# Kernel tuning notes

Hardware: AMD Instinct MI355X
Metric: run time of the kernel (lower is better)

The kernel has to match this reference:

```python
import jax, jax.numpy as jnp
import numpy as np

OUT_FEAT = 11008
IN_FEAT = 4096
HAD_DIM = 128


def setup_inputs() -> dict:
    key = jax.random.key(0)
    k1, k2, k3 = jax.random.split(key, 3)
    inp = jax.random.normal(k1, (OUT_FEAT, IN_FEAT), dtype=jnp.float32) * 0.02
    # rotation matrices (Hadamard-like random orthogonal stand-ins, scaled)
    R_left = jax.random.normal(k2, (IN_FEAT, IN_FEAT), dtype=jnp.float32) / np.sqrt(IN_FEAT)
    R_right = jax.random.normal(k3, (HAD_DIM, HAD_DIM), dtype=jnp.float32) / np.sqrt(HAD_DIM)
    return {"inp": inp, "R_left": R_left, "R_right": R_right}


def _fake_quant_int8(x):
    # symmetric per-tensor int8 fake quant with straight-through estimator
    scale = jnp.max(jnp.abs(x)) / 127.0
    scale = jnp.maximum(scale, jnp.finfo(x.dtype).tiny)
    q = jnp.clip(jnp.round(x / scale), -127.0, 127.0) * scale
    return x + jax.lax.stop_gradient(q - x)


def reference(inp, R_left, R_right):
    # RotQuantWrapper.forward, branch: R_left is not None, R1_is_left=True, R_right set.
    org_dtype = inp.dtype
    out_feat, in_feat = inp.shape  # inp is W^T: (out_feat, in_feat)
    compute_dtype = jnp.float32
    # inp @ R_left  -> (out_feat, in_feat)
    x = inp.astype(compute_dtype) @ R_left.astype(compute_dtype)
    had_dim = R_right.shape[0]
    # (W^T A)^T -> reshape -> block-multiply by B (had_dim blocks) -> back
    x = x.T  # (in_feat, out_feat)
    x = x.reshape(in_feat, out_feat // had_dim, had_dim)
    x = x @ R_right.astype(compute_dtype)  # batched small matmul over 128-blocks
    x = x.reshape(in_feat, out_feat).T  # (out_feat, in_feat)
    x = x.astype(org_dtype)
    return _fake_quant_int8(x)
```

## Files before the change

kernel.cpp:

```cpp
#include <hip/hip_runtime.h>
#include <hip/hip_fp16.h>

#define OUT_FEAT 11008
#define IN_FEAT  4096
#define HAD      128

typedef __attribute__((ext_vector_type(8))) _Float16 f16x8;
typedef __attribute__((ext_vector_type(4))) float    f32x4;

__device__ __forceinline__ void lds_load16(const _Float16* g, _Float16* l) {
    __builtin_amdgcn_global_load_lds(
        (const __attribute__((address_space(1))) void*)g,
        (__attribute__((address_space(3))) void*)l, 16, 0, 0);
}

__global__ __launch_bounds__(256, 2) void k_prep(const float* __restrict__ Rl,
                                                 const float* __restrict__ Rr,
                                                 const float* __restrict__ inp,
                                                 _Float16* __restrict__ Bt,
                                                 __half* __restrict__ W) {
    __shared__ char smem[65536];
    int bid = blockIdx.x;
    int t   = threadIdx.x;

    if (bid < 4096) {
        float (*tile)[65] = (float(*)[65])smem;
        int n0 = (bid & 63) * 64;
        int k0 = (bid >> 6) * 64;
        int tn = t & 63;
        int tr = t >> 6;
#pragma unroll
        for (int r = 0; r < 16; ++r) {
            int kk = r * 4 + tr;
            tile[kk][tn] = Rl[(size_t)(k0 + kk) * IN_FEAT + n0 + tn];
        }
        __syncthreads();
#pragma unroll
        for (int r = 0; r < 16; ++r) {
            int nn = r * 4 + tr;
            Bt[(size_t)(n0 + nn) * IN_FEAT + k0 + tn] = (_Float16)tile[tn][nn];
        }
        return;
    }

    __half2* sR2 = (__half2*)smem;
    __half2* sX2 = (__half2*)(smem + 32768);
    int rb = bid - 4096;
    int i0 = (rb & 31) * 128;
    int b  = rb >> 5;

#pragma unroll
    for (int r = 0; r < 32; ++r) {
        int idx = r * 256 + t;
        float2 v = *(const float2*)&Rr[(size_t)idx * 2];
        sR2[idx] = __floats2half2_rn(v.x, v.y);
    }
    const float* xsrc = inp + (size_t)b * HAD * IN_FEAT + i0;
#pragma unroll
    for (int r = 0; r < 32; ++r) {
        int idx = r * 256 + t;
        int k = idx >> 6, ip = idx & 63;
        float2 v = *(const float2*)&xsrc[(size_t)k * IN_FEAT + ip * 2];
        sX2[idx] = __floats2half2_rn(v.x, v.y);
    }
    __syncthreads();

    int tx = t & 15, ty = t >> 4;
    __half2 acc2[8][4];
#pragma unroll
    for (int j = 0; j < 8; ++j)
#pragma unroll
        for (int c = 0; c < 4; ++c) acc2[j][c] = __float2half2_rn(0.f);

    for (int k = 0; k < 128; ++k) {
        const __half2* rp = &sR2[k * 64 + ty * 4];
        __half2 rr[4] = {rp[0], rp[1], rp[2], rp[3]};
        const __half2* xp = &sX2[k * 64 + tx * 4];
        __half2 xv[4] = {xp[0], xp[1], xp[2], xp[3]};
#pragma unroll
        for (int q = 0; q < 4; ++q) {
            __half2 rlo = __low2half2(rr[q]);
            __half2 rhi = __high2half2(rr[q]);
#pragma unroll
            for (int c = 0; c < 4; ++c) {
                acc2[2 * q][c]     = __hfma2(rlo, xv[c], acc2[2 * q][c]);
                acc2[2 * q + 1][c] = __hfma2(rhi, xv[c], acc2[2 * q + 1][c]);
            }
        }
    }

#pragma unroll
    for (int jj = 0; jj < 8; ++jj) {
        size_t row = (size_t)(b * HAD + ty * 8 + jj) * IN_FEAT;
        union { __half2 h2[4]; f16x8 v; } u;
#pragma unroll
        for (int c = 0; c < 4; ++c) u.h2[c] = acc2[jj][c];
        *(f16x8*)&W[row + i0 + tx * 8] = u.v;
    }
}

#define BM 256
#define BN 256
#define BK 64
#define NT 64

#define DSA(dst, MH, KS, BUF)                                                 \
  _Pragma("unroll") for (int i_ = 0; i_ < 4; ++i_)                            \
      dst[i_] = *(const f16x8*)(aBase + (BUF)*16384 + ((MH)*4 + i_)*1024 +    \
                                ((KS) ? pk1 : pk0));

#define DSB(dst, KS, BUF)                                                     \
  _Pragma("unroll") for (int i_ = 0; i_ < 4; ++i_)                            \
      dst[i_] = *(const f16x8*)(bBase + (BUF)*16384 + i_*1024 +               \
                                ((KS) ? pk1 : pk0));

#define MFMAQ(AB, ar, br)                                                     \
  _Pragma("unroll") for (int mi_ = 0; mi_ < 4; ++mi_)                         \
  _Pragma("unroll") for (int ni_ = 0; ni_ < 4; ++ni_)                         \
      acc[(AB) + mi_][ni_] = __builtin_amdgcn_mfma_f32_16x16x32_f16(          \
          ar[mi_], br[ni_], acc[(AB) + mi_][ni_], 0, 0, 0);

#define PHEAD __builtin_amdgcn_s_barrier(); __builtin_amdgcn_s_setprio(1);
#define PTAIL __builtin_amdgcn_s_setprio(0); __builtin_amdgcn_s_barrier();

#define KTILE(BUF, MODE)                                                      \
  DSA(a, 0, 0, BUF) DSB(b0, 0, BUF)                                           \
  if ((MODE) >= 1) { lds_load16(pA00, &sA[(BUF)^1][0][dstOff]);               \
                     lds_load16(pA01, &sA[(BUF)^1][0][4096 + dstOff]); }      \
  PHEAD MFMAQ(0, a, b0) PTAIL                                                 \
  DSA(a, 0, 1, BUF) DSB(b1, 1, BUF)                                           \
  if ((MODE) >= 1) { lds_load16(pA10, &sA[(BUF)^1][1][dstOff]);               \
                     lds_load16(pA11, &sA[(BUF)^1][1][4096 + dstOff]);        \
                     pA00 += 64; pA01 += 64; pA10 += 64; pA11 += 64; }        \
  PHEAD MFMAQ(0, a, b1) PTAIL                                                 \
  DSA(a, 1, 0, BUF)                                                           \
  if ((MODE) == 2) { lds_load16(pB00, &sB[(BUF)][0][dstOff]);                 \
                     lds_load16(pB01, &sB[(BUF)][0][4096 + dstOff]); }        \
  PHEAD MFMAQ(4, a, b0) PTAIL                                                 \
  DSA(a, 1, 1, BUF)                                                           \
  if ((MODE) == 2) { lds_load16(pB10, &sB[(BUF)][1][dstOff]);                 \
                     lds_load16(pB11, &sB[(BUF)][1][4096 + dstOff]);          \
                     pB00 += 64; pB01 += 64; pB10 += 64; pB11 += 64; }        \
  __builtin_amdgcn_s_barrier(); __builtin_amdgcn_s_setprio(1);                \
  MFMAQ(4, a, b1)                                                             \
  __builtin_amdgcn_s_setprio(0);                                              \
  if ((MODE) == 2) asm volatile("s_waitcnt vmcnt(4)" ::: "memory");           \
  if ((MODE) == 1) asm volatile("s_waitcnt vmcnt(0)" ::: "memory");           \
  __builtin_amdgcn_s_barrier();

__global__ __launch_bounds__(512, 2) void k_gemm(const _Float16* __restrict__ A,
                                                 const _Float16* __restrict__ B,
                                                 float* __restrict__ Cf,
                                                 _Float16* __restrict__ Ch,
                                                 int zf16,
                                                 unsigned* __restrict__ absmax) {
    __shared__ _Float16 sA[2][2][8192];
    __shared__ _Float16 sB[2][2][8192];

    int obid = blockIdx.x;
    int bid  = (obid & 7) * 86 + (obid >> 3);
    int m0 = (bid >> 4) * BM;
    int n0 = (bid & 15) * BN;

    int t = threadIdx.x, lane = t & 63, wid = t >> 6;
    int wr = wid >> 2, wc = wid & 3;
    int fr = lane & 15, g = lane >> 4;

    int r0 = t >> 3;
    int cs = ((t & 7) ^ (r0 & 7)) * 8;
    size_t so = (size_t)r0 * IN_FEAT + cs;
    const _Float16* pA00 = A + (size_t)m0 * IN_FEAT + so;
    const _Float16* pA01 = pA00 + (size_t)64 * IN_FEAT;
    const _Float16* pA10 = pA00 + (size_t)128 * IN_FEAT;
    const _Float16* pA11 = pA00 + (size_t)192 * IN_FEAT;
    const _Float16* pB00 = B + (size_t)n0 * IN_FEAT + so;
    const _Float16* pB01 = pB00 + (size_t)64 * IN_FEAT;
    const _Float16* pB10 = pB00 + (size_t)128 * IN_FEAT;
    const _Float16* pB11 = pB00 + (size_t)192 * IN_FEAT;
    int dstOff = wid * 512;

    const _Float16* aBase = &sA[0][0][0] + wr * 8192 + fr * 64;
    const _Float16* bBase = &sB[0][0][0] + (wc >> 1) * 8192 + (wc & 1) * 4096 + fr * 64;
    int pk0 = (g ^ (fr & 7)) * 8;
    int pk1 = ((4 | g) ^ (fr & 7)) * 8;

    f32x4 acc[8][4] = {};
    f16x8 a[4], b0[4], b1[4];

    lds_load16(pB00, &sB[0][0][dstOff]); lds_load16(pB01, &sB[0][0][4096 + dstOff]);
    lds_load16(pB10, &sB[0][1][dstOff]); lds_load16(pB11, &sB[0][1][4096 + dstOff]);
    pB00 += 64; pB01 += 64; pB10 += 64; pB11 += 64;
    lds_load16(pA00, &sA[0][0][dstOff]); lds_load16(pA01, &sA[0][0][4096 + dstOff]);
    lds_load16(pA10, &sA[0][1][dstOff]); lds_load16(pA11, &sA[0][1][4096 + dstOff]);
    pA00 += 64; pA01 += 64; pA10 += 64; pA11 += 64;
    lds_load16(pB00, &sB[1][0][dstOff]); lds_load16(pB01, &sB[1][0][4096 + dstOff]);
    lds_load16(pB10, &sB[1][1][dstOff]); lds_load16(pB11, &sB[1][1][4096 + dstOff]);
    pB00 += 64; pB01 += 64; pB10 += 64; pB11 += 64;
    asm volatile("s_waitcnt vmcnt(4)" ::: "memory");
    __builtin_amdgcn_s_barrier();

#pragma unroll 1
    for (int kt = 0; kt < NT - 2; kt += 2) {
        KTILE(0, 2)
        KTILE(1, 2)
    }
    KTILE(0, 1)
    KTILE(1, 0)

    float mx = 0.f;
    if (zf16) {
#pragma unroll
        for (int mi = 0; mi < 8; ++mi) {
            int row_base = m0 + wr * 128 + mi * 16 + g * 4;
#pragma unroll
            for (int ni = 0; ni < 4; ++ni) {
                int col = n0 + wc * 64 + ni * 16 + fr;
#pragma unroll
                for (int r = 0; r < 4; ++r) {
                    _Float16 h = (_Float16)acc[mi][ni][r];
                    mx = fmaxf(mx, fabsf((float)h));
                    Ch[(size_t)(row_base + r) * IN_FEAT + col] = h;
                }
            }
        }
    } else {
#pragma unroll
        for (int mi = 0; mi < 8; ++mi) {
            int row_base = m0 + wr * 128 + mi * 16 + g * 4;
#pragma unroll
            for (int ni = 0; ni < 4; ++ni) {
                int col = n0 + wc * 64 + ni * 16 + fr;
#pragma unroll
                for (int r = 0; r < 4; ++r) {
                    float v = acc[mi][ni][r];
                    mx = fmaxf(mx, fabsf(v));
                    Cf[(size_t)(row_base + r) * IN_FEAT + col] = v;
                }
            }
        }
    }
#pragma unroll
    for (int off = 32; off; off >>= 1) mx = fmaxf(mx, __shfl_xor(mx, off));
    if (lane == 0) atomicMax(absmax, __float_as_uint(mx));
}

__global__ void k_quant_f16(const _Float16* __restrict__ Z, float* __restrict__ out,
                            const unsigned* __restrict__ absmax, int n8) {
    float amax  = __uint_as_float(*absmax);
    float scale = fmaxf(amax / 127.0f, 1.17549435e-38f);
    float inv   = 1.0f / scale;
    int stride = gridDim.x * blockDim.x;
    for (int i = blockIdx.x * blockDim.x + threadIdx.x; i < n8; i += stride) {
        f16x8 v = *(const f16x8*)&Z[(size_t)i * 8];
        float4 o1, o2;
        o1.x = fminf(127.f, fmaxf(-127.f, rintf((float)v[0] * inv))) * scale;
        o1.y = fminf(127.f, fmaxf(-127.f, rintf((float)v[1] * inv))) * scale;
        o1.z = fminf(127.f, fmaxf(-127.f, rintf((float)v[2] * inv))) * scale;
        o1.w = fminf(127.f, fmaxf(-127.f, rintf((float)v[3] * inv))) * scale;
        o2.x = fminf(127.f, fmaxf(-127.f, rintf((float)v[4] * inv))) * scale;
        o2.y = fminf(127.f, fmaxf(-127.f, rintf((float)v[5] * inv))) * scale;
        o2.z = fminf(127.f, fmaxf(-127.f, rintf((float)v[6] * inv))) * scale;
        o2.w = fminf(127.f, fmaxf(-127.f, rintf((float)v[7] * inv))) * scale;
        ((float4*)out)[i * 2]     = o1;
        ((float4*)out)[i * 2 + 1] = o2;
    }
}

__global__ void k_quant_f32(float* __restrict__ C, const unsigned* __restrict__ absmax, int n4) {
    float amax  = __uint_as_float(*absmax);
    float scale = fmaxf(amax / 127.0f, 1.17549435e-38f);
    float inv   = 1.0f / scale;
    int stride = gridDim.x * blockDim.x;
    for (int i = blockIdx.x * blockDim.x + threadIdx.x; i < n4; i += stride) {
        float4 v = ((const float4*)C)[i];
        float4 o;
        o.x = fminf(127.f, fmaxf(-127.f, rintf(v.x * inv))) * scale;
        o.y = fminf(127.f, fmaxf(-127.f, rintf(v.y * inv))) * scale;
        o.z = fminf(127.f, fmaxf(-127.f, rintf(v.z * inv))) * scale;
        o.w = fminf(127.f, fmaxf(-127.f, rintf(v.w * inv))) * scale;
        ((float4*)C)[i] = o;
    }
}

extern "C" void kernel_launch(void* const* d_in, const int* in_sizes, int n_in,
                              void* d_out, int out_size, void* d_ws, size_t ws_size,
                              hipStream_t stream) {
    const float* inp = (const float*)d_in[0];
    const float* Rl  = (const float*)d_in[1];
    const float* Rr  = (const float*)d_in[2];
    float* out = (float*)d_out;

    char* ws = (char*)d_ws;
    const size_t W_BYTES  = (size_t)OUT_FEAT * IN_FEAT * 2;
    const size_t BT_BYTES = (size_t)IN_FEAT * IN_FEAT * 2;
    _Float16* Wh   = (_Float16*)ws;
    _Float16* Bt   = (_Float16*)(ws + W_BYTES);
    unsigned* amax = (unsigned*)(ws + W_BYTES + BT_BYTES);
    _Float16* Zh   = (_Float16*)(ws + W_BYTES + BT_BYTES + 1024);
    size_t needed  = W_BYTES + BT_BYTES + 1024 + W_BYTES;
    int zf16 = (ws_size >= needed) ? 1 : 0;

    hipMemsetAsync(amax, 0, 4, stream);
    k_prep<<<dim3(4096 + 2752), 256, 0, stream>>>(Rl, Rr, inp, Bt, (__half*)Wh);
    k_gemm<<<dim3((OUT_FEAT / BM) * (IN_FEAT / BN)), 512, 0, stream>>>(Wh, Bt, out, Zh, zf16, amax);
    if (zf16) {
        int n8 = OUT_FEAT * IN_FEAT / 8;
        k_quant_f16<<<2048, 256, 0, stream>>>(Zh, out, amax, n8);
    } else {
        int n4 = OUT_FEAT * IN_FEAT / 4;
        k_quant_f32<<<2048, 256, 0, stream>>>(out, amax, n4);
    }
}
```

Before: 591.7 us.

## Replace 256x256 pipelined GEMM tiles with smaller 128x128 tiles for better wave balance

Swaps the 512-thread, 256x256x64 GEMM with its hand-interleaved LDS reads, prefetch and priority scheduling for a simpler 256-thread, 128x128x32 double-buffered kernel with one barrier per k-step. It also changes the LDS swizzle and sets launch bounds to three blocks per CU. The goal is to fix the tail imbalance of 688 large blocks on the CUs and to raise occupancy. The cost is lower data reuse per block, more global/LDS traffic per FLOP, and more frequent synchronisation with less overlap of loads and MFMAs.

New measurement: 689.4 us. +16.5%, slower.

```diff
diff --git a/kernel.cpp b/kernel.cpp
--- a/kernel.cpp
+++ b/kernel.cpp
@@ -99,119 +99,78 @@
     }
 }
 
-#define BM 256
-#define BN 256
-#define BK 64
-#define NT 64
-
-#define DSA(dst, MH, KS, BUF)                                                 \
-  _Pragma("unroll") for (int i_ = 0; i_ < 4; ++i_)                            \
-      dst[i_] = *(const f16x8*)(aBase + (BUF)*16384 + ((MH)*4 + i_)*1024 +    \
-                                ((KS) ? pk1 : pk0));
-
-#define DSB(dst, KS, BUF)                                                     \
-  _Pragma("unroll") for (int i_ = 0; i_ < 4; ++i_)                            \
-      dst[i_] = *(const f16x8*)(bBase + (BUF)*16384 + i_*1024 +               \
-                                ((KS) ? pk1 : pk0));
-
-#define MFMAQ(AB, ar, br)                                                     \
+#define BM 128
+#define BN 128
+#define BK 32
+#define NT 128
+
+#define KS(BUF, DOSTAGE)                                                      \
+  __syncthreads();                                                            \
+  if (DOSTAGE) {                                                              \
+    lds_load16(pA0, &sA[BUF ^ 1][dst0]); lds_load16(pA1, &sA[BUF ^ 1][dst1]); \
+    lds_load16(pB0, &sB[BUF ^ 1][dst0]); lds_load16(pB1, &sB[BUF ^ 1][dst1]); \
+    pA0 += BK; pA1 += BK; pB0 += BK; pB1 += BK;                               \
+  }                                                                           \
+  _Pragma("unroll") for (int i_ = 0; i_ < 4; ++i_) {                          \
+    a[i_] = *(const f16x8*)(aBase + (BUF) * 4096 + i_ * 512);                 \
+    b[i_] = *(const f16x8*)(bBase + (BUF) * 4096 + i_ * 512);                 \
+  }                                                                           \
   _Pragma("unroll") for (int mi_ = 0; mi_ < 4; ++mi_)                         \
   _Pragma("unroll") for (int ni_ = 0; ni_ < 4; ++ni_)                         \
-      acc[(AB) + mi_][ni_] = __builtin_amdgcn_mfma_f32_16x16x32_f16(          \
-          ar[mi_], br[ni_], acc[(AB) + mi_][ni_], 0, 0, 0);
-
-#define PHEAD __builtin_amdgcn_s_barrier(); __builtin_amdgcn_s_setprio(1);
-#define PTAIL __builtin_amdgcn_s_setprio(0); __builtin_amdgcn_s_barrier();
-
-#define KTILE(BUF, MODE)                                                      \
-  DSA(a, 0, 0, BUF) DSB(b0, 0, BUF)                                           \
-  if ((MODE) >= 1) { lds_load16(pA00, &sA[(BUF)^1][0][dstOff]);               \
-                     lds_load16(pA01, &sA[(BUF)^1][0][4096 + dstOff]); }      \
-  PHEAD MFMAQ(0, a, b0) PTAIL                                                 \
-  DSA(a, 0, 1, BUF) DSB(b1, 1, BUF)                                           \
-  if ((MODE) >= 1) { lds_load16(pA10, &sA[(BUF)^1][1][dstOff]);               \
-                     lds_load16(pA11, &sA[(BUF)^1][1][4096 + dstOff]);        \
-                     pA00 += 64; pA01 += 64; pA10 += 64; pA11 += 64; }        \
-  PHEAD MFMAQ(0, a, b1) PTAIL                                                 \
-  DSA(a, 1, 0, BUF)                                                           \
-  if ((MODE) == 2) { lds_load16(pB00, &sB[(BUF)][0][dstOff]);                 \
-                     lds_load16(pB01, &sB[(BUF)][0][4096 + dstOff]); }        \
-  PHEAD MFMAQ(4, a, b0) PTAIL                                                 \
-  DSA(a, 1, 1, BUF)                                                           \
-  if ((MODE) == 2) { lds_load16(pB10, &sB[(BUF)][1][dstOff]);                 \
-                     lds_load16(pB11, &sB[(BUF)][1][4096 + dstOff]);          \
-                     pB00 += 64; pB01 += 64; pB10 += 64; pB11 += 64; }        \
-  __builtin_amdgcn_s_barrier(); __builtin_amdgcn_s_setprio(1);                \
-  MFMAQ(4, a, b1)                                                             \
-  __builtin_amdgcn_s_setprio(0);                                              \
-  if ((MODE) == 2) asm volatile("s_waitcnt vmcnt(4)" ::: "memory");           \
-  if ((MODE) == 1) asm volatile("s_waitcnt vmcnt(0)" ::: "memory");           \
-  __builtin_amdgcn_s_barrier();
-
-__global__ __launch_bounds__(512, 2) void k_gemm(const _Float16* __restrict__ A,
+      acc[mi_][ni_] = __builtin_amdgcn_mfma_f32_16x16x32_f16(                 \
+          a[mi_], b[ni_], acc[mi_][ni_], 0, 0, 0);
+
+__global__ __launch_bounds__(256, 3) void k_gemm(const _Float16* __restrict__ A,
                                                  const _Float16* __restrict__ B,
                                                  float* __restrict__ Cf,
                                                  _Float16* __restrict__ Ch,
                                                  int zf16,
                                                  unsigned* __restrict__ absmax) {
-    __shared__ _Float16 sA[2][2][8192];
-    __shared__ _Float16 sB[2][2][8192];
+    __shared__ _Float16 sA[2][BM * BK];
+    __shared__ _Float16 sB[2][BN * BK];
 
     int obid = blockIdx.x;
-    int bid  = (obid & 7) * 86 + (obid >> 3);
-    int m0 = (bid >> 4) * BM;
-    int n0 = (bid & 15) * BN;
+    int bid  = (obid & 7) * 344 + (obid >> 3);
+    int m0 = (bid >> 5) * BM;
+    int n0 = (bid & 31) * BN;
 
     int t = threadIdx.x, lane = t & 63, wid = t >> 6;
-    int wr = wid >> 2, wc = wid & 3;
+    int wr = wid >> 1, wc = wid & 1;
     int fr = lane & 15, g = lane >> 4;
 
-    int r0 = t >> 3;
-    int cs = ((t & 7) ^ (r0 & 7)) * 8;
-    size_t so = (size_t)r0 * IN_FEAT + cs;
-    const _Float16* pA00 = A + (size_t)m0 * IN_FEAT + so;
-    const _Float16* pA01 = pA00 + (size_t)64 * IN_FEAT;
-    const _Float16* pA10 = pA00 + (size_t)128 * IN_FEAT;
-    const _Float16* pA11 = pA00 + (size_t)192 * IN_FEAT;
-    const _Float16* pB00 = B + (size_t)n0 * IN_FEAT + so;
-    const _Float16* pB01 = pB00 + (size_t)64 * IN_FEAT;
-    const _Float16* pB10 = pB00 + (size_t)128 * IN_FEAT;
-    const _Float16* pB11 = pB00 + (size_t)192 * IN_FEAT;
-    int dstOff = wid * 512;
-
-    const _Float16* aBase = &sA[0][0][0] + wr * 8192 + fr * 64;
-    const _Float16* bBase = &sB[0][0][0] + (wc >> 1) * 8192 + (wc & 1) * 4096 + fr * 64;
-    int pk0 = (g ^ (fr & 7)) * 8;
-    int pk1 = ((4 | g) ^ (fr & 7)) * 8;
-
-    f32x4 acc[8][4] = {};
-    f16x8 a[4], b0[4], b1[4];
-
-    lds_load16(pB00, &sB[0][0][dstOff]); lds_load16(pB01, &sB[0][0][4096 + dstOff]);
-    lds_load16(pB10, &sB[0][1][dstOff]); lds_load16(pB11, &sB[0][1][4096 + dstOff]);
-    pB00 += 64; pB01 += 64; pB10 += 64; pB11 += 64;
-    lds_load16(pA00, &sA[0][0][dstOff]); lds_load16(pA01, &sA[0][0][4096 + dstOff]);
-    lds_load16(pA10, &sA[0][1][dstOff]); lds_load16(pA11, &sA[0][1][4096 + dstOff]);
-    pA00 += 64; pA01 += 64; pA10 += 64; pA11 += 64;
-    lds_load16(pB00, &sB[1][0][dstOff]); lds_load16(pB01, &sB[1][0][4096 + dstOff]);
-    lds_load16(pB10, &sB[1][1][dstOff]); lds_load16(pB11, &sB[1][1][4096 + dstOff]);
-    pB00 += 64; pB01 += 64; pB10 += 64; pB11 += 64;
-    asm volatile("s_waitcnt vmcnt(4)" ::: "memory");
-    __builtin_amdgcn_s_barrier();
+    int srow = t >> 2;
+    int scol = ((t & 3) ^ ((srow >> 1) & 3)) * 8;
+    const _Float16* pA0 = A + (size_t)(m0 + srow) * IN_FEAT + scol;
+    const _Float16* pA1 = pA0 + (size_t)64 * IN_FEAT;
+    const _Float16* pB0 = B + (size_t)(n0 + srow) * IN_FEAT + scol;
+    const _Float16* pB1 = pB0 + (size_t)64 * IN_FEAT;
+    int dst0 = wid * 512;
+    int dst1 = 2048 + wid * 512;
+
+    int pk = (g ^ ((fr >> 1) & 3)) * 8;
+    const _Float16* aBase = &sA[0][0] + (wr * 64 + fr) * BK + pk;
+    const _Float16* bBase = &sB[0][0] + (wc * 64 + fr) * BK + pk;
+
+    f32x4 acc[4][4] = {};
+    f16x8 a[4], b[4];
+
+    lds_load16(pA0, &sA[0][dst0]); lds_load16(pA1, &sA[0][dst1]);
+    lds_load16(pB0, &sB[0][dst0]); lds_load16(pB1, &sB[0][dst1]);
+    pA0 += BK; pA1 += BK; pB0 += BK; pB1 += BK;
 
 #pragma unroll 1
     for (int kt = 0; kt < NT - 2; kt += 2) {
-        KTILE(0, 2)
-        KTILE(1, 2)
-    }
-    KTILE(0, 1)
-    KTILE(1, 0)
+        KS(0, 1)
+        KS(1, 1)
+    }
+    KS(0, 1)
+    KS(1, 0)
 
     float mx = 0.f;
     if (zf16) {
 #pragma unroll
-        for (int mi = 0; mi < 8; ++mi) {
-            int row_base = m0 + wr * 128 + mi * 16 + g * 4;
+        for (int mi = 0; mi < 4; ++mi) {
+            int row_base = m0 + wr * 64 + mi * 16 + g * 4;
 #pragma unroll
             for (int ni = 0; ni < 4; ++ni) {
                 int col = n0 + wc * 64 + ni * 16 + fr;
@@ -225,8 +184,8 @@
         }
     } else {
 #pragma unroll
-        for (int mi = 0; mi < 8; ++mi) {
-            int row_base = m0 + wr * 128 + mi * 16 + g * 4;
+        for (int mi = 0; mi < 4; ++mi) {
+            int row_base = m0 + wr * 64 + mi * 16 + g * 4;
 #pragma unroll
             for (int ni = 0; ni < 4; ++ni) {
                 int col = n0 + wc * 64 + ni * 16 + fr;
@@ -302,7 +261,7 @@
 
     hipMemsetAsync(amax, 0, 4, stream);
     k_prep<<<dim3(4096 + 2752), 256, 0, stream>>>(Rl, Rr, inp, Bt, (__half*)Wh);
-    k_gemm<<<dim3((OUT_FEAT / BM) * (IN_FEAT / BN)), 512, 0, stream>>>(Wh, Bt, out, Zh, zf16, amax);
+    k_gemm<<<dim3((OUT_FEAT / BM) * (IN_FEAT / BN)), 256, 0, stream>>>(Wh, Bt, out, Zh, zf16, amax);
     if (zf16) {
         int n8 = OUT_FEAT * IN_FEAT / 8;
         k_quant_f16<<<2048, 256, 0, stream>>>(Zh, out, amax, n8);
```
